# Optimization experiments

Hardware: AMD Instinct MI355X
Metric: run time of the kernel (lower is better)

The kernel has to match this reference:

```python
import jax, jax.numpy as jnp
import numpy as np

B, S, DIM = 64, 256, 512
H = 16
DH = DIM // H          # 32
W = 256                # window_size == seq_len
ROPE_BASE = 10000.0


def _rope(x):
    # x: (B, S, H, DH), interleaved-pair RoPE
    pos = jnp.arange(S, dtype=jnp.float32)
    inv_freq = 1.0 / (ROPE_BASE ** (jnp.arange(0, DH, 2, dtype=jnp.float32) / DH))
    sinusoid = pos[:, None] * inv_freq[None, :]            # (S, DH/2)
    sin = jnp.sin(sinusoid)[None, :, None, :]              # (1, S, 1, DH/2)
    cos = jnp.cos(sinusoid)[None, :, None, :]
    x1 = x[..., 0::2]
    x2 = x[..., 1::2]
    r1 = x1 * cos - x2 * sin
    r2 = x1 * sin + x2 * cos
    return jnp.stack([r1, r2], axis=-1).reshape(x.shape)


def setup_inputs() -> dict:
    key = jax.random.key(0)
    ks = jax.random.split(key, 8)
    s = 1.0 / np.sqrt(DIM)
    return {
        "hidden_states": jax.random.normal(ks[0], (B, S, DIM), jnp.float32),
        "Wq": jax.random.normal(ks[1], (DIM, DIM), jnp.float32) * s,
        "bq": jnp.zeros((DIM,), jnp.float32),
        "Wk": jax.random.normal(ks[2], (DIM, DIM), jnp.float32) * s,
        "bk": jnp.zeros((DIM,), jnp.float32),
        "Wv": jax.random.normal(ks[3], (DIM, DIM), jnp.float32) * s,
        "bv": jnp.zeros((DIM,), jnp.float32),
        "bias_table": jax.random.normal(ks[4], (2 * W - 1, H), jnp.float32) * 0.02,
    }


def reference(hidden_states, Wq, bq, Wk, bk, Wv, bv, bias_table):
    b, s, _ = hidden_states.shape
    q = hidden_states @ Wq + bq
    k = hidden_states @ Wk + bk
    v = hidden_states @ Wv + bv
    # (B, S, H, DH)
    q = _rope(q.reshape(b, s, H, DH))
    k = _rope(k.reshape(b, s, H, DH))
    v = v.reshape(b, s, H, DH)
    # (B, H, S, DH)
    q = q.transpose(0, 2, 1, 3)
    k = k.transpose(0, 2, 1, 3)
    v = v.transpose(0, 2, 1, 3)
    scores = jnp.einsum('bhqd,bhkd->bhqk', q, k) / np.sqrt(DH)
    # relative_position_index[i, j] == (i - j) + W - 1
    rel_idx = jnp.arange(W)[:, None] - jnp.arange(W)[None, :] + (W - 1)
    rel_bias = bias_table[rel_idx]                 # (W, W, H)
    rel_bias = rel_bias.transpose(2, 0, 1)[None]   # (1, H, W, W)
    # NOTE: bias added AFTER softmax, faithful to the original module
    probs = jax.nn.softmax(scores, axis=-1) + rel_bias
    ctx = jnp.einsum('bhqk,bhkd->bhqd', probs, v)
    ctx = ctx.transpose(0, 2, 1, 3).reshape(b, s, DIM)
    return ctx
```

## Files before the change

### kernel.cpp

```cpp
#include <hip/hip_runtime.h>
#include <stdint.h>

typedef __attribute__((ext_vector_type(8))) short bf16x8;
typedef __attribute__((ext_vector_type(4))) float f32x4;
typedef __attribute__((ext_vector_type(4))) unsigned int u32x4;

#define MFMA16(a, b, c) __builtin_amdgcn_mfma_f32_16x16x32_bf16(a, b, c, 0, 0, 0)

__device__ __forceinline__ float bf2f(unsigned short u) {
    union { unsigned int i; float f; } x; x.i = ((unsigned int)u) << 16; return x.f;
}
__device__ __forceinline__ unsigned short f2bf(float f) {
    union { float f; unsigned int i; } x; x.f = f;
    unsigned int u = x.i;
    return (unsigned short)((u + 0x7FFFu + ((u >> 16) & 1u)) >> 16);
}

__global__ __launch_bounds__(256) void k_cvt(const float4* __restrict__ in,
                                             unsigned short* __restrict__ out) {
    int i = blockIdx.x * 256 + threadIdx.x;
    float4 v = in[i];
    ushort4 o;
    o.x = f2bf(v.x); o.y = f2bf(v.y); o.z = f2bf(v.z); o.w = f2bf(v.w);
    *(ushort4*)(out + (size_t)i * 4) = o;
}

__global__ __launch_bounds__(256) void k_wt(const float* __restrict__ W0,
                                            const float* __restrict__ W1,
                                            const float* __restrict__ W2,
                                            unsigned short* __restrict__ Wt) {
    __shared__ float t[64][65];
    const float* Wm = (blockIdx.z == 0) ? W0 : (blockIdx.z == 1) ? W1 : W2;
    int k0 = blockIdx.x * 64, n0 = blockIdx.y * 64;
    for (int it = 0; it < 16; ++it) {
        int idx = threadIdx.x + it * 256;
        int r = idx >> 6, c = idx & 63;
        t[r][c] = Wm[(k0 + r) * 512 + n0 + c];
    }
    __syncthreads();
    unsigned short* dst = Wt + (size_t)blockIdx.z * 512 * 512;
    for (int it = 0; it < 16; ++it) {
        int idx = threadIdx.x + it * 256;
        int nr = idx >> 6, kc = idx & 63;
        dst[(n0 + nr) * 512 + k0 + kc] = f2bf(t[kc][nr]);
    }
}

__global__ __launch_bounds__(256) void k_sc(float* __restrict__ cs2) {
    int s = threadIdx.x;
    for (int f = 0; f < 16; ++f) {
        float inv = powf(10000.0f, -(float)f / 16.0f);
        float a = (float)s * inv;
        cs2[(s * 16 + f) * 2 + 0] = cosf(a);
        cs2[(s * 16 + f) * 2 + 1] = sinf(a);
    }
}

__global__ __launch_bounds__(256, 2) void k_gemm(
    const unsigned short* __restrict__ A,
    const unsigned short* __restrict__ Bw,
    const float* __restrict__ bq, const float* __restrict__ bk, const float* __restrict__ bv,
    const float* __restrict__ cs2,
    unsigned short* __restrict__ Qo, unsigned short* __restrict__ Ko, unsigned short* __restrict__ Vo) {
    __shared__ unsigned short a_l[2][8192];
    __shared__ unsigned short b_l[2][8192];
    const int tid = threadIdx.x;
    const int wave = tid >> 6, lane = tid & 63;
    const int l15 = lane & 15, l4 = lane >> 4;
    int bid = blockIdx.x;
    int swz = (bid & 7) * 192 + (bid >> 3);
    const int m0 = (swz / 12) * 128;
    const int n0 = (swz % 12) * 128;
    const int wm = (wave >> 1) * 64, wn = (wave & 1) * 64;
    const bool isV = (n0 >= 1024);

    f32x4 zero4 = {0.f, 0.f, 0.f, 0.f};
    f32x4 acc[4][4];
#pragma unroll
    for (int i = 0; i < 4; ++i)
#pragma unroll
        for (int j = 0; j < 4; ++j) acc[i][j] = zero4;

    const int srow = tid >> 3;
    const int skc = ((tid & 7) ^ (srow & 7)) * 8;
    const unsigned short* ga = A + (size_t)(m0 + srow) * 512 + skc;
    const unsigned short* gb = Bw + (size_t)(n0 + srow) * 512 + skc;

#define STAGE(buf, kt)                                                                          \
    {                                                                                           \
        const unsigned short* pa = ga + (kt) * 64;                                              \
        const unsigned short* pb = gb + (kt) * 64;                                              \
        unsigned short* la = &a_l[(buf)][wave * 512];                                           \
        unsigned short* lb = &b_l[(buf)][wave * 512];                                           \
        _Pragma("unroll")                                                                       \
        for (int it = 0; it < 4; ++it) {                                                        \
            __builtin_amdgcn_global_load_lds(                                                   \
                (const __attribute__((address_space(1))) unsigned int*)(pa + it * (32 * 512)),  \
                (__attribute__((address_space(3))) unsigned int*)(la + it * 2048), 16, 0, 0);   \
            __builtin_amdgcn_global_load_lds(                                                   \
                (const __attribute__((address_space(1))) unsigned int*)(pb + it * (32 * 512)),  \
                (__attribute__((address_space(3))) unsigned int*)(lb + it * 2048), 16, 0, 0);   \
        }                                                                                       \
    }

    STAGE(0, 0);
    __syncthreads();
    int cur = 0;
    for (int kt = 0; kt < 8; ++kt) {
        if (kt < 7) STAGE(cur ^ 1, kt + 1);
#pragma unroll
        for (int kc = 0; kc < 2; ++kc) {
            bf16x8 af[4], bfr[4];
#pragma unroll
            for (int i = 0; i < 4; ++i) {
                int g = ((kc * 4 + l4) ^ (l15 & 7)) * 8;
                af[i] = *(const bf16x8*)&a_l[cur][(wm + i * 16 + l15) * 64 + g];
            }
#pragma unroll
            for (int j = 0; j < 4; ++j) {
                int g = ((kc * 4 + l4) ^ (l15 & 7)) * 8;
                bfr[j] = *(const bf16x8*)&b_l[cur][(wn + j * 16 + l15) * 64 + g];
            }
            if (!isV) {
#pragma unroll
                for (int i = 0; i < 4; ++i)
#pragma unroll
                    for (int j = 0; j < 4; ++j) acc[i][j] = MFMA16(af[i], bfr[j], acc[i][j]);
            } else {
#pragma unroll
                for (int i = 0; i < 4; ++i)
#pragma unroll
                    for (int j = 0; j < 4; ++j) acc[i][j] = MFMA16(bfr[j], af[i], acc[i][j]);
            }
        }
        __syncthreads();
        cur ^= 1;
    }
#undef STAGE

    if (!isV) {
        const int mat = n0 >> 9;
        unsigned short* __restrict__ dst = (mat == 0) ? Qo : Ko;
        const float* __restrict__ bias = (mat == 0) ? bq : bk;
#pragma unroll
        for (int j = 0; j < 4; ++j) {
            int col = (n0 & 511) + wn + j * 16 + l15;
            float bb = bias[col];
            int h = col >> 5, dh = col & 31, f = dh >> 1;
            float sgn = (col & 1) ? 1.0f : -1.0f;
#pragma unroll
            for (int i = 0; i < 4; ++i) {
#pragma unroll
                for (int r = 0; r < 4; ++r) {
                    int m = m0 + wm + i * 16 + l4 * 4 + r;
                    int b2 = m >> 8, s = m & 255;
                    float t = acc[i][j][r] + bb;
                    float partner = __shfl_xor(t, 1);
                    float2 cn = *(const float2*)(cs2 + (s * 16 + f) * 2);
                    float o = t * cn.x + sgn * partner * cn.y;
                    dst[(size_t)(b2 * 16 + h) * 8192 + s * 32 + dh] = f2bf(o);
                }
            }
        }
    } else {
#pragma unroll
        for (int j = 0; j < 4; ++j) {
#pragma unroll
            for (int r = 0; r < 4; ++r) {
                int n = (n0 & 511) + wn + j * 16 + l4 * 4 + r;
                float bb = bv[n];
                int h = n >> 5, dh = n & 31;
#pragma unroll
                for (int i = 0; i < 4; ++i) {
                    int m = m0 + wm + i * 16 + l15;
                    int b2 = m >> 8, s = m & 255;
                    Vo[(size_t)(b2 * 16 + h) * 8192 + dh * 256 + s] = f2bf(acc[i][j][r] + bb);
                }
            }
        }
    }
}

__global__ __launch_bounds__(256, 3) void k_attn(
    const unsigned short* __restrict__ Qm, const unsigned short* __restrict__ Km,
    const unsigned short* __restrict__ Vm,
    const float* __restrict__ bias_table, float* __restrict__ out) {
    __shared__ unsigned short k_l[256 * 32];
    __shared__ unsigned short vt_l[32 * 256];
    __shared__ float bias_g[512];

    const int tid = threadIdx.x, wave = tid >> 6, lane = tid & 63;
    const int l15 = lane & 15, l4 = lane >> 4;
    int bid = blockIdx.x;
    int swz = (bid & 7) * 128 + (bid >> 3);
    const int h = swz & 15, b = swz >> 4;
    const size_t bh = ((size_t)(b * 16 + h)) * 8192;

    for (int i = tid; i < 511; i += 256) bias_g[i] = bias_table[i * 16 + h];

#pragma unroll
    for (int it = 0; it < 4; ++it) {
        int p = it * 256 + wave * 64 + lane;
        __builtin_amdgcn_global_load_lds(
            (const __attribute__((address_space(1))) unsigned int*)(Km + bh + p * 8),
            (__attribute__((address_space(3))) unsigned int*)(k_l + it * 2048 + wave * 512), 16, 0, 0);
    }
#pragma unroll
    for (int it = 0; it < 4; ++it) {
        int p = it * 256 + wave * 64 + lane;
        int dh = p >> 5, cpos = p & 31;
        int srcc = cpos ^ (dh & 7);
        __builtin_amdgcn_global_load_lds(
            (const __attribute__((address_space(1))) unsigned int*)(Vm + bh + dh * 256 + srcc * 8),
            (__attribute__((address_space(3))) unsigned int*)(vt_l + it * 2048 + wave * 512), 16, 0, 0);
    }
    __syncthreads();

    f32x4 zero4 = {0.f, 0.f, 0.f, 0.f};
    const float SCL2 = 0.17677669529663687f * 1.4426950408889634f;
    const int qrow = 16 * wave + l15;
    const bool hi = (l4 >> 1) != 0;
    const bool odd = (l4 & 1) != 0;

    for (int qb = 0; qb < 4; ++qb) {
        const int q0 = qb * 64;
        bf16x8 qfrag = *(const bf16x8*)(Qm + bh + (size_t)(q0 + qrow) * 32 + l4 * 8);

        f32x4 sc[16];
#pragma unroll
        for (int ct = 0; ct < 16; ++ct) {
            bf16x8 kf = *(const bf16x8*)&k_l[(ct * 16 + l15) * 32 + l4 * 8];
            sc[ct] = MFMA16(kf, qfrag, zero4);
        }

        float sum = 0.f;
#pragma unroll
        for (int ct = 0; ct < 16; ++ct) {
#pragma unroll
            for (int r = 0; r < 4; ++r) {
                float e;
                float x = sc[ct][r] * SCL2;
                asm("v_exp_f32 %0, %1" : "=v"(e) : "v"(x));
                sc[ct][r] = e;
                sum += e;
            }
        }
        sum += __shfl_xor(sum, 16);
        sum += __shfl_xor(sum, 32);
        float inv = 1.0f / sum;

        f32x4 o0 = zero4, o1 = zero4;
#pragma unroll
        for (int m = 0; m < 8; ++m) {
            unsigned int E0, E1, O0, O1;
            {
                int kbase = 32 * m + 4 * l4;
                int jb = q0 + qrow - kbase + 255;
                float p0 = sc[2 * m][0] * inv + bias_g[jb];
                float p1 = sc[2 * m][1] * inv + bias_g[jb - 1];
                float p2 = sc[2 * m][2] * inv + bias_g[jb - 2];
                float p3 = sc[2 * m][3] * inv + bias_g[jb - 3];
                asm("v_cvt_pk_bf16_f32 %0, %1, %2" : "=v"(E0) : "v"(p0), "v"(p1));
                asm("v_cvt_pk_bf16_f32 %0, %1, %2" : "=v"(E1) : "v"(p2), "v"(p3));
                jb -= 16;
                p0 = sc[2 * m + 1][0] * inv + bias_g[jb];
                p1 = sc[2 * m + 1][1] * inv + bias_g[jb - 1];
                p2 = sc[2 * m + 1][2] * inv + bias_g[jb - 2];
                p3 = sc[2 * m + 1][3] * inv + bias_g[jb - 3];
                asm("v_cvt_pk_bf16_f32 %0, %1, %2" : "=v"(O0) : "v"(p0), "v"(p1));
                asm("v_cvt_pk_bf16_f32 %0, %1, %2" : "=v"(O1) : "v"(p2), "v"(p3));
            }
            unsigned int m0_ = hi ? O0 : E0, m1_ = hi ? O1 : E1;
            unsigned int s0 = hi ? E0 : O0, s1 = hi ? E1 : O1;
            unsigned int g0 = __shfl_xor(s0, 32), g1 = __shfl_xor(s1, 32);
            unsigned int X00 = hi ? g0 : m0_, X01 = hi ? g1 : m1_;
            unsigned int X10 = hi ? m0_ : g0, X11 = hi ? m1_ : g1;
            unsigned int k0 = odd ? X10 : X00, k1 = odd ? X11 : X01;
            unsigned int t0 = odd ? X00 : X10, t1 = odd ? X01 : X11;
            unsigned int r0 = __shfl_xor(t0, 16), r1 = __shfl_xor(t1, 16);
            union { unsigned int u[4]; bf16x8 v; } pu;
            pu.u[0] = odd ? r0 : k0; pu.u[1] = odd ? r1 : k1;
            pu.u[2] = odd ? k0 : r0; pu.u[3] = odd ? k1 : r1;
            int vc = (m * 4 + l4) ^ (l15 & 7);
            bf16x8 v0 = *(const bf16x8*)&vt_l[l15 * 256 + vc * 8];
            bf16x8 v1 = *(const bf16x8*)&vt_l[(16 + l15) * 256 + vc * 8];
            o0 = MFMA16(pu.v, v0, o0);
            o1 = MFMA16(pu.v, v1, o1);
        }

#pragma unroll
        for (int r = 0; r < 4; ++r) {
            int s = q0 + 16 * wave + l4 * 4 + r;
            float* po = out + ((size_t)(b * 256 + s)) * 512 + h * 32;
            po[l15] = o0[r];
            po[16 + l15] = o1[r];
        }
    }
}

extern "C" void kernel_launch(void* const* d_in, const int* in_sizes, int n_in,
                              void* d_out, int out_size, void* d_ws, size_t ws_size,
                              hipStream_t stream) {
    const float* hs = (const float*)d_in[0];
    const float* Wq = (const float*)d_in[1];
    const float* bq = (const float*)d_in[2];
    const float* Wk = (const float*)d_in[3];
    const float* bk = (const float*)d_in[4];
    const float* Wv = (const float*)d_in[5];
    const float* bv = (const float*)d_in[6];
    const float* bt = (const float*)d_in[7];
    float* out = (float*)d_out;

    char* ws = (char*)d_ws;
    unsigned short* hsb = (unsigned short*)ws;
    unsigned short* wt = (unsigned short*)(ws + 16777216);
    unsigned short* Qo = (unsigned short*)(ws + 18350080);
    unsigned short* Ko = (unsigned short*)(ws + 35127296);
    unsigned short* Vo = (unsigned short*)(ws + 51904512);
    float* cs2 = (float*)(ws + 68681728);

    hipLaunchKernelGGL(k_cvt, dim3(8192), dim3(256), 0, stream, (const float4*)hs, hsb);
    hipLaunchKernelGGL(k_wt, dim3(8, 8, 3), dim3(256), 0, stream, Wq, Wk, Wv, wt);
    hipLaunchKernelGGL(k_sc, dim3(1), dim3(256), 0, stream, cs2);
    hipLaunchKernelGGL(k_gemm, dim3(1536), dim3(256), 0, stream,
                       hsb, wt, bq, bk, bv, cs2, Qo, Ko, Vo);
    hipLaunchKernelGGL(k_attn, dim3(1024), dim3(256), 0, stream,
                       Qo, Ko, Vo, bt, out);
}
```

Baseline: 96.47 us.

## Halve GEMM K-tile for higher occupancy; prefetch Q and split softmax sums

Measured after the change: 106.6 us. +10.5%, slower.

```diff
diff --git a/kernel.cpp b/kernel.cpp
--- a/kernel.cpp
+++ b/kernel.cpp
@@ -56,14 +56,14 @@
     }
 }
 
-__global__ __launch_bounds__(256, 2) void k_gemm(
+__global__ __launch_bounds__(256, 3) void k_gemm(
     const unsigned short* __restrict__ A,
     const unsigned short* __restrict__ Bw,
     const float* __restrict__ bq, const float* __restrict__ bk, const float* __restrict__ bv,
     const float* __restrict__ cs2,
     unsigned short* __restrict__ Qo, unsigned short* __restrict__ Ko, unsigned short* __restrict__ Vo) {
-    __shared__ unsigned short a_l[2][8192];
-    __shared__ unsigned short b_l[2][8192];
+    __shared__ unsigned short a_l[2][4096];
+    __shared__ unsigned short b_l[2][4096];
     const int tid = threadIdx.x;
     const int wave = tid >> 6, lane = tid & 63;
     const int l15 = lane & 15, l4 = lane >> 4;
@@ -81,62 +81,55 @@
 #pragma unroll
         for (int j = 0; j < 4; ++j) acc[i][j] = zero4;
 
-    const int srow = tid >> 3;
-    const int skc = ((tid & 7) ^ (srow & 7)) * 8;
-    const unsigned short* ga = A + (size_t)(m0 + srow) * 512 + skc;
-    const unsigned short* gb = Bw + (size_t)(n0 + srow) * 512 + skc;
-
-#define STAGE(buf, kt)                                                                          \
-    {                                                                                           \
-        const unsigned short* pa = ga + (kt) * 64;                                              \
-        const unsigned short* pb = gb + (kt) * 64;                                              \
-        unsigned short* la = &a_l[(buf)][wave * 512];                                           \
-        unsigned short* lb = &b_l[(buf)][wave * 512];                                           \
-        _Pragma("unroll")                                                                       \
-        for (int it = 0; it < 4; ++it) {                                                        \
-            __builtin_amdgcn_global_load_lds(                                                   \
-                (const __attribute__((address_space(1))) unsigned int*)(pa + it * (32 * 512)),  \
-                (__attribute__((address_space(3))) unsigned int*)(la + it * 2048), 16, 0, 0);   \
-            __builtin_amdgcn_global_load_lds(                                                   \
-                (const __attribute__((address_space(1))) unsigned int*)(pb + it * (32 * 512)),  \
-                (__attribute__((address_space(3))) unsigned int*)(lb + it * 2048), 16, 0, 0);   \
-        }                                                                                       \
-    }
+    const int r0 = tid >> 2, c0 = (tid & 3) ^ ((tid >> 3) & 3);
+    const int p1 = tid + 256;
+    const int r1 = p1 >> 2, c1 = (p1 & 3) ^ ((p1 >> 3) & 3);
+    const unsigned short* gA0 = A + (size_t)(m0 + r0) * 512 + c0 * 8;
+    const unsigned short* gA1 = A + (size_t)(m0 + r1) * 512 + c1 * 8;
+    const unsigned short* gB0 = Bw + (size_t)(n0 + r0) * 512 + c0 * 8;
+    const unsigned short* gB1 = Bw + (size_t)(n0 + r1) * 512 + c1 * 8;
+
+#define GLDS(src, dst) __builtin_amdgcn_global_load_lds(                        \
+        (const __attribute__((address_space(1))) unsigned int*)(src),           \
+        (__attribute__((address_space(3))) unsigned int*)(dst), 16, 0, 0)
+#define STAGE(buf, kt)                                                          \
+    {                                                                           \
+        GLDS(gA0 + (kt) * 32, &a_l[(buf)][wave * 512]);                         \
+        GLDS(gA1 + (kt) * 32, &a_l[(buf)][2048 + wave * 512]);                  \
+        GLDS(gB0 + (kt) * 32, &b_l[(buf)][wave * 512]);                         \
+        GLDS(gB1 + (kt) * 32, &b_l[(buf)][2048 + wave * 512]);                  \
+    }
+
+    const int g = (l4 ^ ((l15 >> 1) & 3)) * 8;
 
     STAGE(0, 0);
     __syncthreads();
     int cur = 0;
-    for (int kt = 0; kt < 8; ++kt) {
-        if (kt < 7) STAGE(cur ^ 1, kt + 1);
-#pragma unroll
-        for (int kc = 0; kc < 2; ++kc) {
-            bf16x8 af[4], bfr[4];
-#pragma unroll
-            for (int i = 0; i < 4; ++i) {
-                int g = ((kc * 4 + l4) ^ (l15 & 7)) * 8;
-                af[i] = *(const bf16x8*)&a_l[cur][(wm + i * 16 + l15) * 64 + g];
-            }
-#pragma unroll
-            for (int j = 0; j < 4; ++j) {
-                int g = ((kc * 4 + l4) ^ (l15 & 7)) * 8;
-                bfr[j] = *(const bf16x8*)&b_l[cur][(wn + j * 16 + l15) * 64 + g];
-            }
-            if (!isV) {
-#pragma unroll
-                for (int i = 0; i < 4; ++i)
-#pragma unroll
-                    for (int j = 0; j < 4; ++j) acc[i][j] = MFMA16(af[i], bfr[j], acc[i][j]);
-            } else {
-#pragma unroll
-                for (int i = 0; i < 4; ++i)
-#pragma unroll
-                    for (int j = 0; j < 4; ++j) acc[i][j] = MFMA16(bfr[j], af[i], acc[i][j]);
-            }
+    for (int kt = 0; kt < 16; ++kt) {
+        if (kt < 15) STAGE(cur ^ 1, kt + 1);
+        bf16x8 af[4], bfr[4];
+#pragma unroll
+        for (int i = 0; i < 4; ++i)
+            af[i] = *(const bf16x8*)&a_l[cur][(wm + i * 16 + l15) * 32 + g];
+#pragma unroll
+        for (int j = 0; j < 4; ++j)
+            bfr[j] = *(const bf16x8*)&b_l[cur][(wn + j * 16 + l15) * 32 + g];
+        if (!isV) {
+#pragma unroll
+            for (int i = 0; i < 4; ++i)
+#pragma unroll
+                for (int j = 0; j < 4; ++j) acc[i][j] = MFMA16(af[i], bfr[j], acc[i][j]);
+        } else {
+#pragma unroll
+            for (int i = 0; i < 4; ++i)
+#pragma unroll
+                for (int j = 0; j < 4; ++j) acc[i][j] = MFMA16(bfr[j], af[i], acc[i][j]);
         }
         __syncthreads();
         cur ^= 1;
     }
 #undef STAGE
+#undef GLDS
 
     if (!isV) {
         const int mat = n0 >> 9;
@@ -222,29 +215,35 @@
     const bool hi = (l4 >> 1) != 0;
     const bool odd = (l4 & 1) != 0;
 
+    bf16x8 qcur = *(const bf16x8*)(Qm + bh + (size_t)qrow * 32 + l4 * 8);
+
     for (int qb = 0; qb < 4; ++qb) {
         const int q0 = qb * 64;
-        bf16x8 qfrag = *(const bf16x8*)(Qm + bh + (size_t)(q0 + qrow) * 32 + l4 * 8);
+        bf16x8 qnext;
+        if (qb < 3)
+            qnext = *(const bf16x8*)(Qm + bh + (size_t)(q0 + 64 + qrow) * 32 + l4 * 8);
 
         f32x4 sc[16];
 #pragma unroll
         for (int ct = 0; ct < 16; ++ct) {
             bf16x8 kf = *(const bf16x8*)&k_l[(ct * 16 + l15) * 32 + l4 * 8];
-            sc[ct] = MFMA16(kf, qfrag, zero4);
-        }
-
-        float sum = 0.f;
+            sc[ct] = MFMA16(kf, qcur, zero4);
+        }
+
+        float s0 = 0.f, s1 = 0.f, s2 = 0.f, s3 = 0.f;
 #pragma unroll
         for (int ct = 0; ct < 16; ++ct) {
-#pragma unroll
-            for (int r = 0; r < 4; ++r) {
-                float e;
-                float x = sc[ct][r] * SCL2;
-                asm("v_exp_f32 %0, %1" : "=v"(e) : "v"(x));
-                sc[ct][r] = e;
-                sum += e;
-            }
-        }
+            float e0, e1, e2, e3;
+            float x0 = sc[ct][0] * SCL2, x1 = sc[ct][1] * SCL2;
+            float x2 = sc[ct][2] * SCL2, x3 = sc[ct][3] * SCL2;
+            asm("v_exp_f32 %0, %1" : "=v"(e0) : "v"(x0));
+            asm("v_exp_f32 %0, %1" : "=v"(e1) : "v"(x1));
+            asm("v_exp_f32 %0, %1" : "=v"(e2) : "v"(x2));
+            asm("v_exp_f32 %0, %1" : "=v"(e3) : "v"(x3));
+            sc[ct][0] = e0; sc[ct][1] = e1; sc[ct][2] = e2; sc[ct][3] = e3;
+            s0 += e0; s1 += e1; s2 += e2; s3 += e3;
+        }
+        float sum = (s0 + s1) + (s2 + s3);
         sum += __shfl_xor(sum, 16);
         sum += __shfl_xor(sum, 32);
         float inv = 1.0f / sum;
@@ -271,8 +270,8 @@
                 asm("v_cvt_pk_bf16_f32 %0, %1, %2" : "=v"(O1) : "v"(p2), "v"(p3));
             }
             unsigned int m0_ = hi ? O0 : E0, m1_ = hi ? O1 : E1;
-            unsigned int s0 = hi ? E0 : O0, s1 = hi ? E1 : O1;
-            unsigned int g0 = __shfl_xor(s0, 32), g1 = __shfl_xor(s1, 32);
+            unsigned int s0_ = hi ? E0 : O0, s1_ = hi ? E1 : O1;
+            unsigned int g0 = __shfl_xor(s0_, 32), g1 = __shfl_xor(s1_, 32);
             unsigned int X00 = hi ? g0 : m0_, X01 = hi ? g1 : m1_;
             unsigned int X10 = hi ? m0_ : g0, X11 = hi ? m1_ : g1;
             unsigned int k0 = odd ? X10 : X00, k1 = odd ? X11 : X01;
@@ -295,6 +294,7 @@
             po[l15] = o0[r];
             po[16 + l15] = o1[r];
         }
+        if (qb < 3) qcur = qnext;
     }
 }
 
```

## Deepen GEMM LDS prefetch to two stages and prefetch Q fragments in attention

Applied to the files above, without the earlier changes.

New measurement: 94.82 us. About the same (-1.7%).

```diff
diff --git a/kernel.cpp b/kernel.cpp
--- a/kernel.cpp
+++ b/kernel.cpp
@@ -104,10 +104,12 @@
     }
 
     STAGE(0, 0);
-    __syncthreads();
+    STAGE(1, 1);
     int cur = 0;
     for (int kt = 0; kt < 8; ++kt) {
-        if (kt < 7) STAGE(cur ^ 1, kt + 1);
+        if (kt < 7) { asm volatile("s_waitcnt vmcnt(8)" ::: "memory"); }
+        else        { asm volatile("s_waitcnt vmcnt(0)" ::: "memory"); }
+        __builtin_amdgcn_s_barrier();
 #pragma unroll
         for (int kc = 0; kc < 2; ++kc) {
             bf16x8 af[4], bfr[4];
@@ -133,7 +135,9 @@
                     for (int j = 0; j < 4; ++j) acc[i][j] = MFMA16(bfr[j], af[i], acc[i][j]);
             }
         }
-        __syncthreads();
+        asm volatile("" ::: "memory");
+        __builtin_amdgcn_s_barrier();
+        if (kt < 6) STAGE(cur, kt + 2);
         cur ^= 1;
     }
 #undef STAGE
@@ -222,29 +226,35 @@
     const bool hi = (l4 >> 1) != 0;
     const bool odd = (l4 & 1) != 0;
 
+    bf16x8 qcur = *(const bf16x8*)(Qm + bh + (size_t)qrow * 32 + l4 * 8);
+
     for (int qb = 0; qb < 4; ++qb) {
         const int q0 = qb * 64;
-        bf16x8 qfrag = *(const bf16x8*)(Qm + bh + (size_t)(q0 + qrow) * 32 + l4 * 8);
+        bf16x8 qnext;
+        if (qb < 3)
+            qnext = *(const bf16x8*)(Qm + bh + (size_t)(q0 + 64 + qrow) * 32 + l4 * 8);
 
         f32x4 sc[16];
 #pragma unroll
         for (int ct = 0; ct < 16; ++ct) {
             bf16x8 kf = *(const bf16x8*)&k_l[(ct * 16 + l15) * 32 + l4 * 8];
-            sc[ct] = MFMA16(kf, qfrag, zero4);
-        }
-
-        float sum = 0.f;
+            sc[ct] = MFMA16(kf, qcur, zero4);
+        }
+
+        float s0 = 0.f, s1 = 0.f, s2 = 0.f, s3 = 0.f;
 #pragma unroll
         for (int ct = 0; ct < 16; ++ct) {
-#pragma unroll
-            for (int r = 0; r < 4; ++r) {
-                float e;
-                float x = sc[ct][r] * SCL2;
-                asm("v_exp_f32 %0, %1" : "=v"(e) : "v"(x));
-                sc[ct][r] = e;
-                sum += e;
-            }
-        }
+            float e0, e1, e2, e3;
+            float x0 = sc[ct][0] * SCL2, x1 = sc[ct][1] * SCL2;
+            float x2 = sc[ct][2] * SCL2, x3 = sc[ct][3] * SCL2;
+            asm("v_exp_f32 %0, %1" : "=v"(e0) : "v"(x0));
+            asm("v_exp_f32 %0, %1" : "=v"(e1) : "v"(x1));
+            asm("v_exp_f32 %0, %1" : "=v"(e2) : "v"(x2));
+            asm("v_exp_f32 %0, %1" : "=v"(e3) : "v"(x3));
+            sc[ct][0] = e0; sc[ct][1] = e1; sc[ct][2] = e2; sc[ct][3] = e3;
+            s0 += e0; s1 += e1; s2 += e2; s3 += e3;
+        }
+        float sum = (s0 + s1) + (s2 + s3);
         sum += __shfl_xor(sum, 16);
         sum += __shfl_xor(sum, 32);
         float inv = 1.0f / sum;
@@ -271,8 +281,8 @@
                 asm("v_cvt_pk_bf16_f32 %0, %1, %2" : "=v"(O1) : "v"(p2), "v"(p3));
             }
             unsigned int m0_ = hi ? O0 : E0, m1_ = hi ? O1 : E1;
-            unsigned int s0 = hi ? E0 : O0, s1 = hi ? E1 : O1;
-            unsigned int g0 = __shfl_xor(s0, 32), g1 = __shfl_xor(s1, 32);
+            unsigned int s0_ = hi ? E0 : O0, s1_ = hi ? E1 : O1;
+            unsigned int g0 = __shfl_xor(s0_, 32), g1 = __shfl_xor(s1_, 32);
             unsigned int X00 = hi ? g0 : m0_, X01 = hi ? g1 : m1_;
             unsigned int X10 = hi ? m0_ : g0, X11 = hi ? m1_ : g1;
             unsigned int k0 = odd ? X10 : X00, k1 = odd ? X11 : X01;
@@ -295,6 +305,7 @@
             po[l15] = o0[r];
             po[16 + l15] = o1[r];
         }
+        if (qb < 3) qcur = qnext;
     }
 }
 
```
